# Kernel optimization log

Hardware: AMD Instinct MI355X
Metric: run time of the kernel (lower is better)

The kernel has to match this reference:

```python
import jax, jax.numpy as jnp
import numpy as np

B, S, F, H = 2, 2048, 1024, 16
HD = F // H  # head_dim = 64


def rope_embedding(length: int, features: int) -> jnp.ndarray:
    # Faithful copy of the module's unusual RoPE: emb = concat[sin, cos] used as an
    # elementwise multiplier, with symmetric averaging for positions > 0.
    base = 10000.0
    inv_freq = 1.0 / base ** (jnp.arange(0, features, 2, dtype=jnp.float32) / features)
    sinusoid = jnp.einsum('i,j->ij', jnp.arange(length, dtype=jnp.float32), inv_freq)
    sin = jnp.sin(sinusoid)
    cos = jnp.cos(sinusoid)  # features even, so no trailing-column drop
    emb = jnp.concatenate([sin, cos], axis=1)[:, None, :]  # [L, 1, HD]
    if length > 1:
        emb_sym = (emb[1:] + emb[1:][::-1]) / 2.0
        emb = jnp.concatenate([emb[:1], emb_sym], axis=0)
    return emb


def setup_inputs() -> dict:
    key = jax.random.key(0)
    ks = jax.random.split(key, 6)
    scale = 1.0 / np.sqrt(F)
    kv = jax.random.normal(ks[0], (B, S, F), dtype=jnp.float32)
    q = jax.random.normal(ks[1], (B, S, F), dtype=jnp.float32)
    Wq = jax.random.normal(ks[2], (F, F), dtype=jnp.float32) * scale
    Wk = jax.random.normal(ks[3], (F, F), dtype=jnp.float32) * scale
    Wv = jax.random.normal(ks[4], (F, F), dtype=jnp.float32) * scale
    Wo = jax.random.normal(ks[5], (F, F), dtype=jnp.float32) * scale
    mask = jnp.tril(jnp.ones((S, S), dtype=bool))[None, None]  # causal [1,1,S,S]
    return {"kv": kv, "q": q, "Wq": Wq, "Wk": Wk, "Wv": Wv, "Wo": Wo, "mask": mask}


def reference(kv, q, Wq, Wk, Wv, Wo, mask):
    # Dense projections (use_bias=False)
    query = (q @ Wq).reshape(B, S, H, HD)
    key_ = (kv @ Wk).reshape(B, S, H, HD)
    value = (kv @ Wv).reshape(B, S, H, HD)
    # Inline RoPE multiply (module's variant)
    emb = rope_embedding(S, HD)  # [S, 1, HD]
    query = query * emb
    key_ = key_ * emb
    # Scores [B, H, Sq, Sk], scale, mask, softmax
    aw = jnp.einsum('bqhd,bkhd->bhqk', query, key_) / jnp.sqrt(jnp.float32(HD))
    aw = jnp.where(mask, aw, jnp.finfo(jnp.float32).min)
    aw = jax.nn.softmax(aw, axis=-1)
    out = jnp.einsum('bhqk,bkhd->bqhd', aw, value).reshape(B, S, F)
    return out @ Wo
```

## Files before the change

### kernel.cpp

```cpp
#include <hip/hip_runtime.h>

typedef unsigned short u16;
typedef unsigned int u32;

#define S_LEN 2048
#define FEAT 1024
#define NHEAD 16
#define HDIM 64
#define NBATCH 2
#define NROWS (NBATCH * S_LEN)

typedef float f32x4 __attribute__((ext_vector_type(4)));
typedef short s16x8 __attribute__((ext_vector_type(8)));
typedef u32 u32x2 __attribute__((ext_vector_type(2)));

#define LOG2E 1.4426950408889634f

__device__ inline u16 f2bf(float f) {
  u32 u = __float_as_uint(f);
  return (u16)((u + 0x7fffu + ((u >> 16) & 1u)) >> 16);
}

__device__ inline u32 cvt_pk_bf16(float lo, float hi) {
  u32 r;
  asm("v_cvt_pk_bf16_f32 %0, %1, %2" : "=v"(r) : "v"(lo), "v"(hi));
  return r;
}

__device__ inline float fexp2(float x) { return __builtin_amdgcn_exp2f(x); }

__device__ inline f32x4 mfma16(s16x8 a, s16x8 b, f32x4 c) {
  return __builtin_amdgcn_mfma_f32_16x16x32_bf16(a, b, c, 0, 0, 0);
}

typedef __attribute__((address_space(1))) void gvoid;
typedef __attribute__((address_space(3))) void lvoid;
__device__ inline void gload_lds16(const void* g, void* l) {
  __builtin_amdgcn_global_load_lds((gvoid*)g, (lvoid*)l, 16, 0, 0);
}

__device__ inline int swz64(int p) { return p ^ (((p >> 7) & 7) << 4); }

struct us4 { u16 x, y, z, w; };
__global__ __launch_bounds__(256) void prep_kernel(
    const float* __restrict__ q, const float* __restrict__ kv,
    const float* __restrict__ Wq, const float* __restrict__ Wk,
    const float* __restrict__ Wv, const float* __restrict__ Wo,
    u16* __restrict__ qbf, u16* __restrict__ kvbf,
    u16* __restrict__ WqT, u16* __restrict__ WkT,
    u16* __restrict__ WvT, u16* __restrict__ WoT,
    float* __restrict__ emb) {
  __shared__ float tile[32][33];
  int bid = blockIdx.x, tid = threadIdx.x;
  const int n4each = NROWS * FEAT / 4;
  if (bid < 8192) {
    int i = bid * 256 + tid;
    const float* in = q;
    u16* out = qbf;
    if (i >= n4each) { i -= n4each; in = kv; out = kvbf; }
    float4 v = ((const float4*)in)[i];
    us4 o;
    o.x = f2bf(v.x); o.y = f2bf(v.y); o.z = f2bf(v.z); o.w = f2bf(v.w);
    ((us4*)out)[i] = o;
  } else if (bid < 12288) {
    int idx = bid - 8192;
    int z = idx >> 10, rem = idx & 1023;
    int by = rem >> 5, bx = rem & 31;
    const float* W = z == 0 ? Wq : z == 1 ? Wk : z == 2 ? Wv : Wo;
    u16* O = z == 0 ? WqT : z == 1 ? WkT : z == 2 ? WvT : WoT;
    int tx = tid & 31, ty = tid >> 5;
    int bi = bx * 32, bo = by * 32;
#pragma unroll
    for (int r = 0; r < 32; r += 8) tile[ty + r][tx] = W[(bi + ty + r) * FEAT + bo + tx];
    __syncthreads();
#pragma unroll
    for (int r = 0; r < 32; r += 8) O[(bo + ty + r) * FEAT + bi + tx] = f2bf(tile[tx][ty + r]);
  } else {
    int i = (bid - 12288) * 256 + tid;
    if (i >= S_LEN * HDIM) return;
    int p = i >> 6, d = i & 63, j = d & 31;
    float invf = exp2f(-13.287712379549449f * (float)j / 32.0f);
    float a1 = (float)p * invf;
    float v1 = (d < 32) ? sinf(a1) : cosf(a1);
    float e;
    if (p == 0) {
      e = v1;
    } else {
      float a2 = (float)(S_LEN - p) * invf;
      float v2 = (d < 32) ? sinf(a2) : cosf(a2);
      e = 0.5f * (v1 + v2);
    }
    emb[i] = e;
  }
}

__global__ __launch_bounds__(256, 3) void gemm_qkv(
    const u16* __restrict__ qbf, const u16* __restrict__ kvbf,
    const u16* __restrict__ WqT, const u16* __restrict__ WkT, const u16* __restrict__ WvT,
    u16* __restrict__ Qb, u16* __restrict__ Kx, u16* __restrict__ Vx,
    const float* __restrict__ emb) {
  __shared__ __align__(16) u16 lA[3][128 * 32];
  __shared__ __align__(16) u16 lB[3][128 * 32];
  const int K = FEAT;
  int t = threadIdx.x;
  int w = t >> 6, l = t & 63;
  int lr = l & 15, lk = l >> 4;
  int flat = blockIdx.y * 32 + blockIdx.x;
  int xcd = flat & 7, idx = flat >> 3;
  int cx = xcd & 3, cy = xcd >> 2;
  int bx = cx * 8 + (idx & 7);
  int yy = cy * 12 + (idx >> 3);
  int mode = yy >> 3;
  int row0 = bx * 128, col0 = (yy & 7) * 128;
  int wm = w >> 1, wn = w & 1;

  const u16* A = mode == 0 ? qbf : kvbf;
  const u16* Bt = mode == 0 ? WqT : mode == 1 ? WkT : WvT;
  u16* Out = mode == 0 ? Qb : mode == 1 ? Kx : Vx;

  f32x4 acc[4][4] = {};

  int P0 = t * 16, P1 = P0 + 4096;
  int L0 = swz64(P0), L1 = swz64(P1);
  const char* Ab = (const char*)A;
  const char* Bb = (const char*)Bt;
  size_t aOff0 = (size_t)(row0 + (L0 >> 6)) * (K * 2) + (L0 & 63);
  size_t aOff1 = (size_t)(row0 + (L1 >> 6)) * (K * 2) + (L1 & 63);
  size_t bOff0 = (size_t)(col0 + (L0 >> 6)) * (K * 2) + (L0 & 63);
  size_t bOff1 = (size_t)(col0 + (L1 >> 6)) * (K * 2) + (L1 & 63);

  auto stage = [&](int buf, int kt) {
    int kb = kt * 64;
    gload_lds16(Ab + aOff0 + kb, (char*)&lA[buf][0] + w * 1024);
    gload_lds16(Ab + aOff1 + kb, (char*)&lA[buf][0] + w * 1024 + 4096);
    gload_lds16(Bb + bOff0 + kb, (char*)&lB[buf][0] + w * 1024);
    gload_lds16(Bb + bOff1 + kb, (char*)&lB[buf][0] + w * 1024 + 4096);
  };

  stage(0, 0);
  const int NK = K / 32;
  int bufc = 0;
  for (int kt = 0; kt < NK; ++kt) {
    int nb3 = (bufc == 2) ? 0 : bufc + 1;
    if (kt + 1 < NK) {
      stage(nb3, kt + 1);
      asm volatile("s_waitcnt vmcnt(4)" ::: "memory");
    } else {
      asm volatile("s_waitcnt vmcnt(0)" ::: "memory");
    }
    __builtin_amdgcn_s_barrier();

    const char* la = (const char*)&lA[bufc][0];
    const char* lb = (const char*)&lB[bufc][0];
    s16x8 af[4], bfr[4];
#pragma unroll
    for (int mi = 0; mi < 4; ++mi) {
      int byte = (wm * 64 + mi * 16 + lr) * 64 + lk * 16;
      af[mi] = *(const s16x8*)(la + swz64(byte));
    }
#pragma unroll
    for (int ni = 0; ni < 4; ++ni) {
      int byte = (wn * 64 + ni * 16 + lr) * 64 + lk * 16;
      bfr[ni] = *(const s16x8*)(lb + swz64(byte));
    }
    __builtin_amdgcn_s_setprio(1);
#pragma unroll
    for (int mi = 0; mi < 4; ++mi)
#pragma unroll
      for (int ni = 0; ni < 4; ++ni)
        acc[mi][ni] = mfma16(af[mi], bfr[ni], acc[mi][ni]);
    __builtin_amdgcn_s_setprio(0);
    bufc = nb3;
  }

  int rb = row0 + wm * 64 + lk * 4;
  int cb = col0 + wn * 64 + lr;
#pragma unroll
  for (int mi = 0; mi < 4; ++mi)
#pragma unroll
    for (int ni = 0; ni < 4; ++ni) {
      int col = cb + ni * 16;
      int h = col >> 6, d = col & (HDIM - 1);
      if (mode <= 1) {
#pragma unroll
        for (int r = 0; r < 4; ++r) {
          int row = rb + mi * 16 + r;
          int b = row >> 11, s = row & (S_LEN - 1);
          float v = acc[mi][ni][r] * emb[s * HDIM + d];
          if (mode == 0) v *= 0.125f;
          Out[(((b << 4) + h) * S_LEN + s) * HDIM + d] = f2bf(v);
        }
      } else {
        int s0 = rb + mi * 16;
        int b = s0 >> 11, s = s0 & (S_LEN - 1);
        us4 o;
        o.x = f2bf(acc[mi][ni][0]); o.y = f2bf(acc[mi][ni][1]);
        o.z = f2bf(acc[mi][ni][2]); o.w = f2bf(acc[mi][ni][3]);
        *(us4*)&Out[(((b << 4) + h) * HDIM + d) * S_LEN + s] = o;
      }
    }
}

__global__ __launch_bounds__(256, 2) void gemm_oproj(
    const u16* __restrict__ A, const u16* __restrict__ Bt, float* __restrict__ Out) {
  __shared__ __align__(16) u16 lA[3][128 * 32];
  __shared__ __align__(16) u16 lB[3][64 * 32];
  const int K = FEAT, N = FEAT;
  int t = threadIdx.x;
  int w = t >> 6, l = t & 63;
  int lr = l & 15, lk = l >> 4;
  int flat = blockIdx.y * 32 + blockIdx.x;
  int xcd = flat & 7, idx = flat >> 3;
  int cx = xcd & 3, cy = xcd >> 2;
  int bx = cx * 8 + (idx & 7);
  int by = cy * 8 + (idx >> 3);
  int row0 = bx * 128, col0 = by * 64;
  int wm = w >> 1, wn = w & 1;

  f32x4 acc[4][2] = {};

  int P0 = t * 16, P1 = P0 + 4096;
  int L0 = swz64(P0), L1 = swz64(P1);
  const char* Ab = (const char*)A;
  const char* Bb = (const char*)Bt;
  size_t aOff0 = (size_t)(row0 + (L0 >> 6)) * (K * 2) + (L0 & 63);
  size_t aOff1 = (size_t)(row0 + (L1 >> 6)) * (K * 2) + (L1 & 63);
  size_t bOff0 = (size_t)(col0 + (L0 >> 6)) * (K * 2) + (L0 & 63);

  auto stage = [&](int buf, int kt) {
    int kb = kt * 64;
    gload_lds16(Ab + aOff0 + kb, (char*)&lA[buf][0] + w * 1024);
    gload_lds16(Ab + aOff1 + kb, (char*)&lA[buf][0] + w * 1024 + 4096);
    gload_lds16(Bb + bOff0 + kb, (char*)&lB[buf][0] + w * 1024);
  };

  stage(0, 0);
  const int NK = K / 32;
  int bufc = 0;
  for (int kt = 0; kt < NK; ++kt) {
    int nb3 = (bufc == 2) ? 0 : bufc + 1;
    if (kt + 1 < NK) {
      stage(nb3, kt + 1);
      asm volatile("s_waitcnt vmcnt(3)" ::: "memory");
    } else {
      asm volatile("s_waitcnt vmcnt(0)" ::: "memory");
    }
    __builtin_amdgcn_s_barrier();

    const char* la = (const char*)&lA[bufc][0];
    const char* lb = (const char*)&lB[bufc][0];
    s16x8 af[4], bfr[2];
#pragma unroll
    for (int mi = 0; mi < 4; ++mi) {
      int byte = (wm * 64 + mi * 16 + lr) * 64 + lk * 16;
      af[mi] = *(const s16x8*)(la + swz64(byte));
    }
#pragma unroll
    for (int ni = 0; ni < 2; ++ni) {
      int byte = (wn * 32 + ni * 16 + lr) * 64 + lk * 16;
      bfr[ni] = *(const s16x8*)(lb + swz64(byte));
    }
    __builtin_amdgcn_s_setprio(1);
#pragma unroll
    for (int mi = 0; mi < 4; ++mi)
#pragma unroll
      for (int ni = 0; ni < 2; ++ni)
        acc[mi][ni] = mfma16(af[mi], bfr[ni], acc[mi][ni]);
    __builtin_amdgcn_s_setprio(0);
    bufc = nb3;
  }

  int rb = row0 + wm * 64 + lk * 4;
  int cb = col0 + wn * 32 + lr;
#pragma unroll
  for (int mi = 0; mi < 4; ++mi)
#pragma unroll
    for (int ni = 0; ni < 2; ++ni)
#pragma unroll
      for (int r = 0; r < 4; ++r)
        Out[(rb + mi * 16 + r) * N + cb + ni * 16] = acc[mi][ni][r];
}

__global__ __launch_bounds__(256, 2) void attn_kernel(
    const u16* __restrict__ Q, const u16* __restrict__ Kb,
    const u16* __restrict__ Vt, u16* __restrict__ AO) {
  __shared__ __align__(16) u16 lK[3][64 * 64];
  __shared__ __align__(16) u16 lV[3][64 * 64];
  __shared__ __align__(16) u16 lP[4][16 * 64];

  int t = threadIdx.x, w = t >> 6, l = t & 63;
  int lr = l & 15, lk = l >> 4;
  int bid = blockIdx.x;
  int xcd = bid & 7, idx = bid >> 3;
  int bh = xcd * 4 + (idx >> 4), qbp = idx & 15;
  int qtA = qbp, qtB = 31 - qbp;
  int ntA = qtA + 1, ntB = qtB + 1;
  const u16* Qp = Q + bh * (S_LEN * HDIM);
  const char* Kc = (const char*)(Kb + bh * (S_LEN * HDIM));
  const char* Vc = (const char*)(Vt + bh * (HDIM * S_LEN));
  int b = bh >> 4, h = bh & 15;
  int sw = (lr & 7) << 4;

  int P0 = w * 1024 + l * 16;
  int row0 = P0 >> 7;
  int srcK0 = P0 ^ ((row0 & 7) << 4);
  int srcV0 = row0 * 4096 + ((P0 & 127) ^ ((row0 & 7) << 4));

  auto stage = [&](int buf, int kt) {
    gload_lds16(Kc + kt * 8192 + srcK0,          (char*)&lK[buf][0] + w * 1024);
    gload_lds16(Kc + kt * 8192 + srcK0 + 4096,   (char*)&lK[buf][0] + w * 1024 + 4096);
    gload_lds16(Vc + kt * 128 + srcV0,           (char*)&lV[buf][0] + w * 1024);
    gload_lds16(Vc + kt * 128 + srcV0 + 131072,  (char*)&lV[buf][0] + w * 1024 + 4096);
  };

  int qrowA = qtA * 64 + w * 16 + lr;
  int qrowB = qtB * 64 + w * 16 + lr;
  s16x8 qA0 = *(const s16x8*)&Qp[qrowA * HDIM + lk * 8];
  s16x8 qA1 = *(const s16x8*)&Qp[qrowA * HDIM + lk * 8 + 32];
  s16x8 qB0 = *(const s16x8*)&Qp[qrowB * HDIM + lk * 8];
  s16x8 qB1 = *(const s16x8*)&Qp[qrowB * HDIM + lk * 8 + 32];

  f32x4 oA[4] = {}, oB[4] = {};
  float lsA = 0.f, lsB = 0.f;
  char* plb = (char*)&lP[w][0];

  auto half_sm_pv = [&](f32x4 (&sacc)[4], f32x4 (&oacc)[4], float& ls,
                        int qrow, bool diag, int kt, const s16x8 (&vf)[4][2]) {
    if (diag) {
#pragma unroll
      for (int nb = 0; nb < 4; ++nb)
#pragma unroll
        for (int r = 0; r < 4; ++r)
          if (kt * 64 + nb * 16 + lk * 4 + r > qrow) sacc[nb][r] = -3.0e38f;
    }
    float rs = 0.f;
    float p[4][4];
#pragma unroll
    for (int nb = 0; nb < 4; ++nb)
#pragma unroll
      for (int r = 0; r < 4; ++r) {
        float pv = fexp2((sacc[nb][r] - 8.0f) * LOG2E);
        p[nb][r] = pv;
        rs += pv;
      }
    ls += rs;
#pragma unroll
    for (int nb = 0; nb < 4; ++nb) {
      u32x2 pw;
      pw.x = cvt_pk_bf16(p[nb][0], p[nb][1]);
      pw.y = cvt_pk_bf16(p[nb][2], p[nb][3]);
      int off = (lr * 128 + nb * 32 + lk * 8) ^ sw;
      *(u32x2*)(plb + off) = pw;
    }
    asm volatile("s_waitcnt lgkmcnt(0)" ::: "memory");
    __builtin_amdgcn_sched_barrier(0);
    s16x8 pf0 = *(const s16x8*)(plb + ((lr * 128 + lk * 16) ^ sw));
    s16x8 pf1 = *(const s16x8*)(plb + ((lr * 128 + 64 + lk * 16) ^ sw));
    __builtin_amdgcn_s_setprio(1);
#pragma unroll
    for (int nd = 0; nd < 4; ++nd) {
      oacc[nd] = mfma16(vf[nd][0], pf0, oacc[nd]);
      oacc[nd] = mfma16(vf[nd][1], pf1, oacc[nd]);
    }
    __builtin_amdgcn_s_setprio(0);
  };

  stage(0, 0);
  int bufc = 0;
  const int NT = 33;
  for (int g = 0; g < NT; ++g) {
    int nb3 = (bufc == 2) ? 0 : bufc + 1;
    if (g + 1 < NT) {
      int g1 = g + 1;
      int kt1 = (g1 >= ntA) ? g1 - ntA : g1;
      stage(nb3, kt1);
      asm volatile("s_waitcnt vmcnt(4)" ::: "memory");
    } else {
      asm volatile("s_waitcnt vmcnt(0)" ::: "memory");
    }
    __builtin_amdgcn_s_barrier();

    bool hB = (g >= ntA);
    int kt = hB ? g - ntA : g;
    const char* kb = (const char*)&lK[bufc][0];
    const char* vb = (const char*)&lV[bufc][0];

    s16x8 vf[4][2];
#pragma unroll
    for (int nd = 0; nd < 4; ++nd)
#pragma unroll
      for (int ks = 0; ks < 2; ++ks)
        vf[nd][ks] = *(const s16x8*)(vb + nd * 2048 + lr * 128 + ((lk * 16 + ks * 64) ^ sw));

    s16x8 q0s = hB ? qB0 : qA0;
    s16x8 q1s = hB ? qB1 : qA1;
    f32x4 s4[4] = {};
    __builtin_amdgcn_s_setprio(1);
#pragma unroll
    for (int nb = 0; nb < 4; ++nb)
#pragma unroll
      for (int ks = 0; ks < 2; ++ks) {
        s16x8 kf = *(const s16x8*)(kb + nb * 2048 + lr * 128 + ((lk * 16 + ks * 64) ^ sw));
        s4[nb] = mfma16(kf, ks ? q1s : q0s, s4[nb]);
      }
    __builtin_amdgcn_s_setprio(0);

    if (hB) half_sm_pv(s4, oB, lsB, qrowB, kt == ntB - 1, kt, vf);
    else    half_sm_pv(s4, oA, lsA, qrowA, kt == ntA - 1, kt, vf);

    bufc = nb3;
  }

  lsA += __shfl_xor(lsA, 16, 64);
  lsA += __shfl_xor(lsA, 32, 64);
  lsB += __shfl_xor(lsB, 16, 64);
  lsB += __shfl_xor(lsB, 32, 64);
#pragma unroll
  for (int half = 0; half < 2; ++half) {
    f32x4* oacc = half ? oB : oA;
    float inv = 1.0f / (half ? lsB : lsA);
    int qrow = half ? qrowB : qrowA;
    u16* dst = &AO[(b * S_LEN + qrow) * FEAT + h * HDIM + lk * 4];
#pragma unroll
    for (int nd = 0; nd < 4; ++nd) {
      us4 o;
      o.x = f2bf(oacc[nd][0] * inv);
      o.y = f2bf(oacc[nd][1] * inv);
      o.z = f2bf(oacc[nd][2] * inv);
      o.w = f2bf(oacc[nd][3] * inv);
      *(us4*)(dst + nd * 16) = o;
    }
  }
}

extern "C" void kernel_launch(void* const* d_in, const int* in_sizes, int n_in,
                              void* d_out, int out_size, void* d_ws, size_t ws_size,
                              hipStream_t stream) {
  const float* kv = (const float*)d_in[0];
  const float* q  = (const float*)d_in[1];
  const float* Wq = (const float*)d_in[2];
  const float* Wk = (const float*)d_in[3];
  const float* Wv = (const float*)d_in[4];
  const float* Wo = (const float*)d_in[5];

  float* emb = (float*)d_ws;
  u16* qbf  = (u16*)((char*)d_ws + S_LEN * HDIM * 4);
  u16* kvbf = qbf + NROWS * FEAT;
  u16* WqT  = kvbf + NROWS * FEAT;
  u16* WkT  = WqT + FEAT * FEAT;
  u16* WvT  = WkT + FEAT * FEAT;
  u16* WoT  = WvT + FEAT * FEAT;
  u16* Qb   = WoT + FEAT * FEAT;
  u16* Kx   = Qb + NROWS * FEAT;
  u16* Vx   = Kx + NROWS * FEAT;
  u16* AO   = Vx + NROWS * FEAT;

  prep_kernel<<<12800, 256, 0, stream>>>(q, kv, Wq, Wk, Wv, Wo,
                                         qbf, kvbf, WqT, WkT, WvT, WoT, emb);

  gemm_qkv<<<dim3(NROWS / 128, 24), 256, 0, stream>>>(qbf, kvbf, WqT, WkT, WvT,
                                                      Qb, Kx, Vx, emb);

  attn_kernel<<<512, 256, 0, stream>>>(Qb, Kx, Vx, AO);

  gemm_oproj<<<dim3(NROWS / 128, FEAT / 64), 256, 0, stream>>>(AO, WoT, (float*)d_out);
}
```

Baseline: 107.8 us.

## Fuse fp32-to-bf16 activation conversion into QKV GEMM A-tile loading

Removes the separate pass that converted q and kv activations to bf16 in the prep kernel. The QKV GEMM now loads the fp32 A tiles into registers, converts them with packed bf16 conversion and writes them to swizzled LDS, prefetching two tiles ahead while B still uses direct global-to-LDS loads. This saves a full read and write of both activation tensors, at the cost of twice the A-side global traffic inside the GEMM, which is read once per column block, plus extra register and VALU work in the main loop.

Result: faster. 105.4 us (-2.2%).

```diff
diff --git a/kernel.cpp b/kernel.cpp
--- a/kernel.cpp
+++ b/kernel.cpp
@@ -13,6 +13,7 @@
 typedef float f32x4 __attribute__((ext_vector_type(4)));
 typedef short s16x8 __attribute__((ext_vector_type(8)));
 typedef u32 u32x2 __attribute__((ext_vector_type(2)));
+typedef u32 u32x4 __attribute__((ext_vector_type(4)));
 
 #define LOG2E 1.4426950408889634f
 
@@ -43,28 +44,15 @@
 
 struct us4 { u16 x, y, z, w; };
 __global__ __launch_bounds__(256) void prep_kernel(
-    const float* __restrict__ q, const float* __restrict__ kv,
     const float* __restrict__ Wq, const float* __restrict__ Wk,
     const float* __restrict__ Wv, const float* __restrict__ Wo,
-    u16* __restrict__ qbf, u16* __restrict__ kvbf,
     u16* __restrict__ WqT, u16* __restrict__ WkT,
     u16* __restrict__ WvT, u16* __restrict__ WoT,
     float* __restrict__ emb) {
   __shared__ float tile[32][33];
   int bid = blockIdx.x, tid = threadIdx.x;
-  const int n4each = NROWS * FEAT / 4;
-  if (bid < 8192) {
-    int i = bid * 256 + tid;
-    const float* in = q;
-    u16* out = qbf;
-    if (i >= n4each) { i -= n4each; in = kv; out = kvbf; }
-    float4 v = ((const float4*)in)[i];
-    us4 o;
-    o.x = f2bf(v.x); o.y = f2bf(v.y); o.z = f2bf(v.z); o.w = f2bf(v.w);
-    ((us4*)out)[i] = o;
-  } else if (bid < 12288) {
-    int idx = bid - 8192;
-    int z = idx >> 10, rem = idx & 1023;
+  if (bid < 4096) {
+    int z = bid >> 10, rem = bid & 1023;
     int by = rem >> 5, bx = rem & 31;
     const float* W = z == 0 ? Wq : z == 1 ? Wk : z == 2 ? Wv : Wo;
     u16* O = z == 0 ? WqT : z == 1 ? WkT : z == 2 ? WvT : WoT;
@@ -76,7 +64,7 @@
 #pragma unroll
     for (int r = 0; r < 32; r += 8) O[(bo + ty + r) * FEAT + bi + tx] = f2bf(tile[tx][ty + r]);
   } else {
-    int i = (bid - 12288) * 256 + tid;
+    int i = (bid - 4096) * 256 + tid;
     if (i >= S_LEN * HDIM) return;
     int p = i >> 6, d = i & 63, j = d & 31;
     float invf = exp2f(-13.287712379549449f * (float)j / 32.0f);
@@ -95,7 +83,7 @@
 }
 
 __global__ __launch_bounds__(256, 3) void gemm_qkv(
-    const u16* __restrict__ qbf, const u16* __restrict__ kvbf,
+    const float* __restrict__ qf, const float* __restrict__ kvf,
     const u16* __restrict__ WqT, const u16* __restrict__ WkT, const u16* __restrict__ WvT,
     u16* __restrict__ Qb, u16* __restrict__ Kx, u16* __restrict__ Vx,
     const float* __restrict__ emb) {
@@ -114,42 +102,59 @@
   int row0 = bx * 128, col0 = (yy & 7) * 128;
   int wm = w >> 1, wn = w & 1;
 
-  const u16* A = mode == 0 ? qbf : kvbf;
+  const float* Af = mode == 0 ? qf : kvf;
   const u16* Bt = mode == 0 ? WqT : mode == 1 ? WkT : WvT;
   u16* Out = mode == 0 ? Qb : mode == 1 ? Kx : Vx;
 
   f32x4 acc[4][4] = {};
 
+  int ar = t >> 2, ac = t & 3;
+  const float* aSrc0 = Af + (size_t)(row0 + ar) * K + ac * 8;
+  const float* aSrc1 = aSrc0 + (size_t)64 * K;
+  int dL0 = swz64(ar * 64 + ac * 16);
+  int dL1 = swz64(ar * 64 + ac * 16 + 4096);
+
   int P0 = t * 16, P1 = P0 + 4096;
   int L0 = swz64(P0), L1 = swz64(P1);
-  const char* Ab = (const char*)A;
   const char* Bb = (const char*)Bt;
-  size_t aOff0 = (size_t)(row0 + (L0 >> 6)) * (K * 2) + (L0 & 63);
-  size_t aOff1 = (size_t)(row0 + (L1 >> 6)) * (K * 2) + (L1 & 63);
   size_t bOff0 = (size_t)(col0 + (L0 >> 6)) * (K * 2) + (L0 & 63);
   size_t bOff1 = (size_t)(col0 + (L1 >> 6)) * (K * 2) + (L1 & 63);
 
-  auto stage = [&](int buf, int kt) {
+  float4 avn[4];
+  auto loadA = [&](int kt) {
+    const float* s0 = aSrc0 + kt * 32;
+    const float* s1 = aSrc1 + kt * 32;
+    avn[0] = *(const float4*)s0; avn[1] = *(const float4*)(s0 + 4);
+    avn[2] = *(const float4*)s1; avn[3] = *(const float4*)(s1 + 4);
+  };
+  auto writeA = [&](int buf) {
+    u32x4 d0, d1;
+    d0.x = cvt_pk_bf16(avn[0].x, avn[0].y); d0.y = cvt_pk_bf16(avn[0].z, avn[0].w);
+    d0.z = cvt_pk_bf16(avn[1].x, avn[1].y); d0.w = cvt_pk_bf16(avn[1].z, avn[1].w);
+    d1.x = cvt_pk_bf16(avn[2].x, avn[2].y); d1.y = cvt_pk_bf16(avn[2].z, avn[2].w);
+    d1.z = cvt_pk_bf16(avn[3].x, avn[3].y); d1.w = cvt_pk_bf16(avn[3].z, avn[3].w);
+    *(u32x4*)((char*)&lA[buf][0] + dL0) = d0;
+    *(u32x4*)((char*)&lA[buf][0] + dL1) = d1;
+  };
+  auto stageB = [&](int buf, int kt) {
     int kb = kt * 64;
-    gload_lds16(Ab + aOff0 + kb, (char*)&lA[buf][0] + w * 1024);
-    gload_lds16(Ab + aOff1 + kb, (char*)&lA[buf][0] + w * 1024 + 4096);
     gload_lds16(Bb + bOff0 + kb, (char*)&lB[buf][0] + w * 1024);
     gload_lds16(Bb + bOff1 + kb, (char*)&lB[buf][0] + w * 1024 + 4096);
   };
 
-  stage(0, 0);
+  loadA(0);
+  stageB(0, 0);
+  asm volatile("s_waitcnt vmcnt(2)" ::: "memory");
+  writeA(0);
+  loadA(1);
+  stageB(1, 1);
+  asm volatile("s_waitcnt vmcnt(6)" ::: "memory");
+  asm volatile("s_waitcnt lgkmcnt(0)" ::: "memory");
+  __builtin_amdgcn_s_barrier();
+
   const int NK = K / 32;
   int bufc = 0;
   for (int kt = 0; kt < NK; ++kt) {
-    int nb3 = (bufc == 2) ? 0 : bufc + 1;
-    if (kt + 1 < NK) {
-      stage(nb3, kt + 1);
-      asm volatile("s_waitcnt vmcnt(4)" ::: "memory");
-    } else {
-      asm volatile("s_waitcnt vmcnt(0)" ::: "memory");
-    }
-    __builtin_amdgcn_s_barrier();
-
     const char* la = (const char*)&lA[bufc][0];
     const char* lb = (const char*)&lB[bufc][0];
     s16x8 af[4], bfr[4];
@@ -170,7 +175,23 @@
       for (int ni = 0; ni < 4; ++ni)
         acc[mi][ni] = mfma16(af[mi], bfr[ni], acc[mi][ni]);
     __builtin_amdgcn_s_setprio(0);
-    bufc = nb3;
+
+    int b1 = (bufc == 2) ? 0 : bufc + 1;
+    int b2 = (b1 == 2) ? 0 : b1 + 1;
+    if (kt + 1 < NK) {
+      asm volatile("s_waitcnt vmcnt(2)" ::: "memory");
+      writeA(b1);
+      if (kt + 2 < NK) {
+        loadA(kt + 2);
+        stageB(b2, kt + 2);
+        asm volatile("s_waitcnt vmcnt(6)" ::: "memory");
+      } else {
+        asm volatile("s_waitcnt vmcnt(0)" ::: "memory");
+      }
+      asm volatile("s_waitcnt lgkmcnt(0)" ::: "memory");
+      __builtin_amdgcn_s_barrier();
+    }
+    bufc = b1;
   }
 
   int rb = row0 + wm * 64 + lk * 4;
@@ -444,9 +465,7 @@
   const float* Wo = (const float*)d_in[5];
 
   float* emb = (float*)d_ws;
-  u16* qbf  = (u16*)((char*)d_ws + S_LEN * HDIM * 4);
-  u16* kvbf = qbf + NROWS * FEAT;
-  u16* WqT  = kvbf + NROWS * FEAT;
+  u16* WqT  = (u16*)((char*)d_ws + S_LEN * HDIM * 4);
   u16* WkT  = WqT + FEAT * FEAT;
   u16* WvT  = WkT + FEAT * FEAT;
   u16* WoT  = WvT + FEAT * FEAT;
@@ -455,10 +474,9 @@
   u16* Vx   = Kx + NROWS * FEAT;
   u16* AO   = Vx + NROWS * FEAT;
 
-  prep_kernel<<<12800, 256, 0, stream>>>(q, kv, Wq, Wk, Wv, Wo,
-                                         qbf, kvbf, WqT, WkT, WvT, WoT, emb);
-
-  gemm_qkv<<<dim3(NROWS / 128, 24), 256, 0, stream>>>(qbf, kvbf, WqT, WkT, WvT,
+  prep_kernel<<<4608, 256, 0, stream>>>(Wq, Wk, Wv, Wo, WqT, WkT, WvT, WoT, emb);
+
+  gemm_qkv<<<dim3(NROWS / 128, 24), 256, 0, stream>>>(q, kv, WqT, WkT, WvT,
                                                       Qb, Kx, Vx, emb);
 
   attn_kernel<<<512, 256, 0, stream>>>(Qb, Kx, Vx, AO);
```

## Split paired causal q-tiles into one tile per block with double buffering

Applied to the files above, without the earlier changes.

The attention kernel used to process two complementary query tiles per block (tile i and 31-i) so every block did the same 33 iterations. It now runs one query tile per block with 1024 blocks, ordered so short and long tiles interleave. K/V staging drops from triple to double buffering to cut LDS use, and launch bounds are raised to 4 blocks per CU for more occupancy. The trade-off is uneven per-block work, which leaves load balance to the hardware scheduler, plus a full vmcnt wait and barrier every iteration with less prefetch depth.

New measurement: 105.9 us. No clear change (-1.7%).

```diff
diff --git a/kernel.cpp b/kernel.cpp
--- a/kernel.cpp
+++ b/kernel.cpp
@@ -281,20 +281,24 @@
         Out[(rb + mi * 16 + r) * N + cb + ni * 16] = acc[mi][ni][r];
 }
 
-__global__ __launch_bounds__(256, 2) void attn_kernel(
+__global__ __launch_bounds__(256, 4) void attn_kernel(
     const u16* __restrict__ Q, const u16* __restrict__ Kb,
     const u16* __restrict__ Vt, u16* __restrict__ AO) {
-  __shared__ __align__(16) u16 lK[3][64 * 64];
-  __shared__ __align__(16) u16 lV[3][64 * 64];
+  __shared__ __align__(16) u16 lK[2][64 * 64];
+  __shared__ __align__(16) u16 lV[2][64 * 64];
   __shared__ __align__(16) u16 lP[4][16 * 64];
 
   int t = threadIdx.x, w = t >> 6, l = t & 63;
   int lr = l & 15, lk = l >> 4;
   int bid = blockIdx.x;
-  int xcd = bid & 7, idx = bid >> 3;
-  int bh = xcd * 4 + (idx >> 4), qbp = idx & 15;
-  int qtA = qbp, qtB = 31 - qbp;
-  int ntA = qtA + 1, ntB = qtB + 1;
+  int xcd = bid & 7, r = bid >> 3;
+  int bh = xcd * 4 + (r & 3);
+  int s = r >> 2;
+  int qt = (s < 8) ? 2 * s
+         : (s < 16) ? 2 * (s - 8) + 1
+         : (s < 24) ? 31 - 2 * (s - 16)
+         : 30 - 2 * (s - 24);
+  int nt = qt + 1;
   const u16* Qp = Q + bh * (S_LEN * HDIM);
   const char* Kc = (const char*)(Kb + bh * (S_LEN * HDIM));
   const char* Vc = (const char*)(Vt + bh * (HDIM * S_LEN));
@@ -313,34 +317,57 @@
     gload_lds16(Vc + kt * 128 + srcV0 + 131072,  (char*)&lV[buf][0] + w * 1024 + 4096);
   };
 
-  int qrowA = qtA * 64 + w * 16 + lr;
-  int qrowB = qtB * 64 + w * 16 + lr;
-  s16x8 qA0 = *(const s16x8*)&Qp[qrowA * HDIM + lk * 8];
-  s16x8 qA1 = *(const s16x8*)&Qp[qrowA * HDIM + lk * 8 + 32];
-  s16x8 qB0 = *(const s16x8*)&Qp[qrowB * HDIM + lk * 8];
-  s16x8 qB1 = *(const s16x8*)&Qp[qrowB * HDIM + lk * 8 + 32];
-
-  f32x4 oA[4] = {}, oB[4] = {};
-  float lsA = 0.f, lsB = 0.f;
+  int qrow = qt * 64 + w * 16 + lr;
+  s16x8 q0 = *(const s16x8*)&Qp[qrow * HDIM + lk * 8];
+  s16x8 q1 = *(const s16x8*)&Qp[qrow * HDIM + lk * 8 + 32];
+
+  f32x4 oacc[4] = {};
+  float ls = 0.f;
   char* plb = (char*)&lP[w][0];
 
-  auto half_sm_pv = [&](f32x4 (&sacc)[4], f32x4 (&oacc)[4], float& ls,
-                        int qrow, bool diag, int kt, const s16x8 (&vf)[4][2]) {
-    if (diag) {
+  stage(0, 0);
+  asm volatile("s_waitcnt vmcnt(0)" ::: "memory");
+  __builtin_amdgcn_s_barrier();
+  int buf = 0;
+  for (int g = 0; g < nt; ++g) {
+    if (g + 1 < nt) stage(buf ^ 1, g + 1);
+    const char* kb = (const char*)&lK[buf][0];
+    const char* vb = (const char*)&lV[buf][0];
+
+    s16x8 vf[4][2];
+#pragma unroll
+    for (int nd = 0; nd < 4; ++nd)
+#pragma unroll
+      for (int ks = 0; ks < 2; ++ks)
+        vf[nd][ks] = *(const s16x8*)(vb + nd * 2048 + lr * 128 + ((lk * 16 + ks * 64) ^ sw));
+
+    f32x4 s4[4] = {};
+    __builtin_amdgcn_s_setprio(1);
+#pragma unroll
+    for (int nb = 0; nb < 4; ++nb)
+#pragma unroll
+      for (int ks = 0; ks < 2; ++ks) {
+        s16x8 kf = *(const s16x8*)(kb + nb * 2048 + lr * 128 + ((lk * 16 + ks * 64) ^ sw));
+        s4[nb] = mfma16(kf, ks ? q1 : q0, s4[nb]);
+      }
+    __builtin_amdgcn_s_setprio(0);
+
+    if (g == nt - 1) {
 #pragma unroll
       for (int nb = 0; nb < 4; ++nb)
 #pragma unroll
-        for (int r = 0; r < 4; ++r)
-          if (kt * 64 + nb * 16 + lk * 4 + r > qrow) sacc[nb][r] = -3.0e38f;
-    }
+        for (int rr = 0; rr < 4; ++rr)
+          if (g * 64 + nb * 16 + lk * 4 + rr > qrow) s4[nb][rr] = -3.0e38f;
+    }
+
     float rs = 0.f;
     float p[4][4];
 #pragma unroll
     for (int nb = 0; nb < 4; ++nb)
 #pragma unroll
-      for (int r = 0; r < 4; ++r) {
-        float pv = fexp2((sacc[nb][r] - 8.0f) * LOG2E);
-        p[nb][r] = pv;
+      for (int rr = 0; rr < 4; ++rr) {
+        float pv = fexp2((s4[nb][rr] - 8.0f) * LOG2E);
+        p[nb][rr] = pv;
         rs += pv;
       }
     ls += rs;
@@ -363,73 +390,26 @@
       oacc[nd] = mfma16(vf[nd][1], pf1, oacc[nd]);
     }
     __builtin_amdgcn_s_setprio(0);
-  };
-
-  stage(0, 0);
-  int bufc = 0;
-  const int NT = 33;
-  for (int g = 0; g < NT; ++g) {
-    int nb3 = (bufc == 2) ? 0 : bufc + 1;
-    if (g + 1 < NT) {
-      int g1 = g + 1;
-      int kt1 = (g1 >= ntA) ? g1 - ntA : g1;
-      stage(nb3, kt1);
-      asm volatile("s_waitcnt vmcnt(4)" ::: "memory");
-    } else {
+
+    if (g + 1 < nt) {
       asm volatile("s_waitcnt vmcnt(0)" ::: "memory");
-    }
-    __builtin_amdgcn_s_barrier();
-
-    bool hB = (g >= ntA);
-    int kt = hB ? g - ntA : g;
-    const char* kb = (const char*)&lK[bufc][0];
-    const char* vb = (const char*)&lV[bufc][0];
-
-    s16x8 vf[4][2];
-#pragma unroll
-    for (int nd = 0; nd < 4; ++nd)
-#pragma unroll
-      for (int ks = 0; ks < 2; ++ks)
-        vf[nd][ks] = *(const s16x8*)(vb + nd * 2048 + lr * 128 + ((lk * 16 + ks * 64) ^ sw));
-
-    s16x8 q0s = hB ? qB0 : qA0;
-    s16x8 q1s = hB ? qB1 : qA1;
-    f32x4 s4[4] = {};
-    __builtin_amdgcn_s_setprio(1);
-#pragma unroll
-    for (int nb = 0; nb < 4; ++nb)
-#pragma unroll
-      for (int ks = 0; ks < 2; ++ks) {
-        s16x8 kf = *(const s16x8*)(kb + nb * 2048 + lr * 128 + ((lk * 16 + ks * 64) ^ sw));
-        s4[nb] = mfma16(kf, ks ? q1s : q0s, s4[nb]);
-      }
-    __builtin_amdgcn_s_setprio(0);
-
-    if (hB) half_sm_pv(s4, oB, lsB, qrowB, kt == ntB - 1, kt, vf);
-    else    half_sm_pv(s4, oA, lsA, qrowA, kt == ntA - 1, kt, vf);
-
-    bufc = nb3;
+      __builtin_amdgcn_s_barrier();
+    }
+    buf ^= 1;
   }
 
-  lsA += __shfl_xor(lsA, 16, 64);
-  lsA += __shfl_xor(lsA, 32, 64);
-  lsB += __shfl_xor(lsB, 16, 64);
-  lsB += __shfl_xor(lsB, 32, 64);
-#pragma unroll
-  for (int half = 0; half < 2; ++half) {
-    f32x4* oacc = half ? oB : oA;
-    float inv = 1.0f / (half ? lsB : lsA);
-    int qrow = half ? qrowB : qrowA;
-    u16* dst = &AO[(b * S_LEN + qrow) * FEAT + h * HDIM + lk * 4];
-#pragma unroll
-    for (int nd = 0; nd < 4; ++nd) {
-      us4 o;
-      o.x = f2bf(oacc[nd][0] * inv);
-      o.y = f2bf(oacc[nd][1] * inv);
-      o.z = f2bf(oacc[nd][2] * inv);
-      o.w = f2bf(oacc[nd][3] * inv);
-      *(us4*)(dst + nd * 16) = o;
-    }
+  ls += __shfl_xor(ls, 16, 64);
+  ls += __shfl_xor(ls, 32, 64);
+  float inv = 1.0f / ls;
+  u16* dst = &AO[(b * S_LEN + qrow) * FEAT + h * HDIM + lk * 4];
+#pragma unroll
+  for (int nd = 0; nd < 4; ++nd) {
+    us4 o;
+    o.x = f2bf(oacc[nd][0] * inv);
+    o.y = f2bf(oacc[nd][1] * inv);
+    o.z = f2bf(oacc[nd][2] * inv);
+    o.w = f2bf(oacc[nd][3] * inv);
+    *(us4*)(dst + nd * 16) = o;
   }
 }
 
@@ -461,7 +441,7 @@
   gemm_qkv<<<dim3(NROWS / 128, 24), 256, 0, stream>>>(qbf, kvbf, WqT, WkT, WvT,
                                                       Qb, Kx, Vx, emb);
 
-  attn_kernel<<<512, 256, 0, stream>>>(Qb, Kx, Vx, AO);
+  attn_kernel<<<1024, 256, 0, stream>>>(Qb, Kx, Vx, AO);
 
   gemm_oproj<<<dim3(NROWS / 128, FEAT / 64), 256, 0, stream>>>(AO, WoT, (float*)d_out);
 }
```
